# Kernel optimization log

Measured on AMD Instinct MI355X. Metric: run time of the kernel, lower is better.

Reference implementation:

```python
import jax, jax.numpy as jnp
import numpy as np

B = 32; D = 512; NH = 8; DH = 64; DEPTH = 8; MLP = 2048
NC = 256; Hs = 16; Ws = 16; SHIFT = 1
INNER = NH * DH


def setup_inputs() -> dict:
    key = jax.random.key(0)
    ks = jax.random.split(key, 8)
    s = D ** -0.5
    return {
        "z": jax.random.normal(ks[0], (B, D, Hs, Ws), jnp.float32),
        "slots": jax.random.normal(ks[1], (B, NC, D), jnp.float32),
        "pos_emb": jax.random.normal(ks[2], (1, Hs * Ws, D), jnp.float32) * s,
        "slot_pos_emb": jax.random.normal(ks[3], (1, NC, D), jnp.float32) * s,
        "norm_w": jnp.ones((D,), jnp.float32),
        "norm_b": jnp.zeros((D,), jnp.float32),
        "ln1_w": jnp.ones((DEPTH, D), jnp.float32),
        "ln1_b": jnp.zeros((DEPTH, D), jnp.float32),
        "qkv_w": jax.random.normal(ks[4], (DEPTH, D, 3 * INNER), jnp.float32) * 0.02,
        "out_w": jax.random.normal(ks[5], (DEPTH, INNER, D), jnp.float32) * 0.02,
        "out_b": jnp.zeros((DEPTH, D), jnp.float32),
        "ln2_w": jnp.ones((DEPTH, D), jnp.float32),
        "ln2_b": jnp.zeros((DEPTH, D), jnp.float32),
        "mlp_w1": jax.random.normal(ks[6], (DEPTH, D, MLP), jnp.float32) * 0.02,
        "mlp_b1": jnp.zeros((DEPTH, MLP), jnp.float32),
        "mlp_w2": jax.random.normal(ks[7], (DEPTH, MLP, D), jnp.float32) * 0.02,
        "mlp_b2": jnp.zeros((DEPTH, D), jnp.float32),
    }


def _ln(x, w, b):
    m = x.mean(-1, keepdims=True)
    v = ((x - m) ** 2).mean(-1, keepdims=True)
    return (x - m) * jax.lax.rsqrt(v + 1e-5) * w + b


def reference(z, slots, pos_emb, slot_pos_emb, norm_w, norm_b,
              ln1_w, ln1_b, qkv_w, out_w, out_b,
              ln2_w, ln2_b, mlp_w1, mlp_b1, mlp_w2, mlp_b2):
    S = NC + Hs * Ws  # 512 tokens: carriers then patches
    mem = slots + slot_pos_emb                                   # [B, NC, D]
    h = z.reshape(B, D, Hs * Ws).transpose(0, 2, 1) + pos_emb    # [B, HW, D]
    x = jnp.concatenate([mem, h], axis=1)                        # [B, S, D]
    x = _ln(x, norm_w, norm_b)
    causal = jnp.tril(jnp.ones((S, S), dtype=bool))              # allowed positions
    scale = DH ** -0.5
    for i in range(DEPTH):
        y = _ln(x, ln1_w[i], ln1_b[i])
        qkv = y @ qkv_w[i]                                       # [B, S, 3*INNER]
        q, k, v = jnp.split(qkv, 3, axis=-1)
        q = q.reshape(B, S, NH, DH).transpose(0, 2, 1, 3)
        k = k.reshape(B, S, NH, DH).transpose(0, 2, 1, 3)
        v = v.reshape(B, S, NH, DH).transpose(0, 2, 1, 3)
        att = jnp.einsum('bhqd,bhkd->bhqk', q, k) * scale
        att = jnp.where(causal, att, jnp.float32(-1e30))
        att = jax.nn.softmax(att, axis=-1)
        o = jnp.einsum('bhqk,bhkd->bhqd', att, v)
        o = o.transpose(0, 2, 1, 3).reshape(B, S, INNER)
        x = x + o @ out_w[i] + out_b[i]
        y = _ln(x, ln2_w[i], ln2_b[i])
        x = x + jax.nn.gelu(y @ mlp_w1[i] + mlp_b1[i], approximate=False) @ mlp_w2[i] + mlp_b2[i]
    out = x[:, NC - SHIFT:NC - SHIFT + Hs * Ws]                  # shifted slice
    return out.transpose(0, 2, 1).reshape(B, D, Hs, Ws)
```

## Files before the change

kernel.cpp:

```cpp
#include <hip/hip_runtime.h>
#include <hip/hip_bf16.h>
#include <math.h>

#define Bb 32
#define Dd 512
#define Ss 512
#define NHh 8
#define DHh 64
#define MLPm 2048
#define NCc 256
#define INNERi 512
#define Mrows (Bb*Ss)

typedef __bf16 bf16x8 __attribute__((ext_vector_type(8)));
typedef float floatx4 __attribute__((ext_vector_type(4)));

__device__ __forceinline__ void load_lds16(const void* g, void* l) {
  __builtin_amdgcn_global_load_lds(
      (__attribute__((address_space(1))) void*)(g),
      (__attribute__((address_space(3))) void*)(l), 16, 0, 0);
}

__device__ __forceinline__ int swz(int row, int seg) {
  return row * 64 + (((seg) ^ (row & 7)) << 3);
}

__global__ void transpose_w(const float* __restrict__ in, __hip_bfloat16* __restrict__ out,
                            int K, int N, size_t in_ls, size_t out_ls)
{
  __shared__ float tile[32][33];
  in  += (size_t)blockIdx.z * in_ls;
  out += (size_t)blockIdx.z * out_ls;
  int n0 = blockIdx.x * 32, k0 = blockIdx.y * 32;
  int tx = threadIdx.x;
  #pragma unroll
  for (int i = threadIdx.y; i < 32; i += 8)
    tile[i][tx] = in[(size_t)(k0 + i) * N + n0 + tx];
  __syncthreads();
  #pragma unroll
  for (int i = threadIdx.y; i < 32; i += 8)
    out[(size_t)(n0 + i) * K + k0 + tx] = __float2bfloat16(tile[tx][i]);
}

__global__ void prologue_kernel(const float* __restrict__ z, const float* __restrict__ slots,
                                const float* __restrict__ pos, const float* __restrict__ spos,
                                const float* __restrict__ nw, const float* __restrict__ nb,
                                float* __restrict__ x)
{
  int row = blockIdx.x;
  int b = row >> 9, s = row & 511;
  int lane = threadIdx.x;
  float v[8];
  float sum = 0.f;
  #pragma unroll
  for (int j = 0; j < 8; ++j) {
    int d = lane + j * 64;
    float t;
    if (s < NCc) t = slots[((size_t)b * NCc + s) * Dd + d] + spos[(size_t)s * Dd + d];
    else {
      int sp = s - NCc;
      t = z[((size_t)b * Dd + d) * 256 + sp] + pos[(size_t)sp * Dd + d];
    }
    v[j] = t; sum += t;
  }
  #pragma unroll
  for (int o = 32; o; o >>= 1) sum += __shfl_xor(sum, o);
  float mean = sum * (1.f / Dd);
  float vs = 0.f;
  #pragma unroll
  for (int j = 0; j < 8; ++j) { float d = v[j] - mean; vs += d * d; }
  #pragma unroll
  for (int o = 32; o; o >>= 1) vs += __shfl_xor(vs, o);
  float rs = rsqrtf(vs * (1.f / Dd) + 1e-5f);
  #pragma unroll
  for (int j = 0; j < 8; ++j) {
    int d = lane + j * 64;
    x[(size_t)row * Dd + d] = (v[j] - mean) * rs * nw[d] + nb[d];
  }
}

__global__ void ln_kernel(const float* __restrict__ x, const float* __restrict__ w,
                          const float* __restrict__ b, __hip_bfloat16* __restrict__ y)
{
  int row = blockIdx.x * 4 + (threadIdx.x >> 6);
  int lane = threadIdx.x & 63;
  const float* xr = x + (size_t)row * Dd;
  float v[8];
  float sum = 0.f;
  #pragma unroll
  for (int j = 0; j < 8; ++j) { v[j] = xr[lane + j * 64]; sum += v[j]; }
  #pragma unroll
  for (int o = 32; o; o >>= 1) sum += __shfl_xor(sum, o);
  float mean = sum * (1.f / Dd);
  float vs = 0.f;
  #pragma unroll
  for (int j = 0; j < 8; ++j) { float d = v[j] - mean; vs += d * d; }
  #pragma unroll
  for (int o = 32; o; o >>= 1) vs += __shfl_xor(vs, o);
  float rs = rsqrtf(vs * (1.f / Dd) + 1e-5f);
  #pragma unroll
  for (int j = 0; j < 8; ++j) {
    int d = lane + j * 64;
    y[(size_t)row * Dd + d] = __float2bfloat16((v[j] - mean) * rs * w[d] + b[d]);
  }
}

template <int MODE>
__global__ __launch_bounds__(256, 2)
void gemm_bt(const __hip_bfloat16* __restrict__ A, const __hip_bfloat16* __restrict__ Bt,
             const float* __restrict__ bias, const float* __restrict__ res,
             void* __restrict__ Out, int M, int N, int K)
{
  constexpr int BM = 128, BN = 128, BK = 64;
  __shared__ __align__(16) __hip_bfloat16 As[BM * BK];
  __shared__ __align__(16) __hip_bfloat16 Bs[BN * BK];
  const int tid = threadIdx.x;
  const int lane = tid & 63;
  const int wave = tid >> 6;

  const int NBLK = N >> 7;
  const int bid = blockIdx.x;
  const int xcd = bid & 7;
  const int j = bid >> 3;
  const int nb = j % NBLK;
  const int mt = xcd + ((j / NBLK) << 3);
  const int m0 = mt << 7;
  const int n0 = nb << 7;

  const int wm = (wave & 1) * 64;
  const int wn = (wave >> 1) * 64;
  const int quad = lane >> 4;
  const int lrow = lane & 15;

  floatx4 acc[4][4];
  #pragma unroll
  for (int i = 0; i < 4; ++i)
    #pragma unroll
    for (int jj = 0; jj < 4; ++jj) {
      floatx4 z4 = {0.f, 0.f, 0.f, 0.f};
      acc[i][jj] = z4;
    }

  for (int k0 = 0; k0 < K; k0 += BK) {
    #pragma unroll
    for (int it = 0; it < 4; ++it) {
      int c = it * 256 + tid;
      int row = c >> 3, seg = (c & 7) ^ (row & 7);
      load_lds16(A + (size_t)(m0 + row) * K + k0 + seg * 8, As + c * 8);
    }
    #pragma unroll
    for (int it = 0; it < 4; ++it) {
      int c = it * 256 + tid;
      int row = c >> 3, seg = (c & 7) ^ (row & 7);
      load_lds16(Bt + (size_t)(n0 + row) * K + k0 + seg * 8, Bs + c * 8);
    }
    __syncthreads();

    #pragma unroll
    for (int k1 = 0; k1 < BK; k1 += 32) {
      const int s0 = k1 >> 3;
      bf16x8 a[4], b[4];
      #pragma unroll
      for (int i = 0; i < 4; ++i)
        a[i] = *reinterpret_cast<const bf16x8*>(&As[swz(wm + i * 16 + lrow, s0 + quad)]);
      #pragma unroll
      for (int i = 0; i < 4; ++i)
        b[i] = *reinterpret_cast<const bf16x8*>(&Bs[swz(wn + i * 16 + lrow, s0 + quad)]);
      #pragma unroll
      for (int mi = 0; mi < 4; ++mi)
        #pragma unroll
        for (int ni = 0; ni < 4; ++ni)
          acc[mi][ni] = __builtin_amdgcn_mfma_f32_16x16x32_bf16(a[mi], b[ni], acc[mi][ni], 0, 0, 0);
    }
    __syncthreads();
  }

  #pragma unroll
  for (int mi = 0; mi < 4; ++mi) {
    #pragma unroll
    for (int r = 0; r < 4; ++r) {
      int gm = m0 + wm + mi * 16 + quad * 4 + r;
      #pragma unroll
      for (int ni = 0; ni < 4; ++ni) {
        int gn = n0 + wn + ni * 16 + lrow;
        float v = acc[mi][ni][r];
        size_t oi = (size_t)gm * N + gn;
        if (MODE == 0) {
          ((__hip_bfloat16*)Out)[oi] = __float2bfloat16(v);
        } else if (MODE == 1) {
          ((float*)Out)[oi] = v + bias[gn] + res[oi];
        } else {
          float t = v + bias[gn];
          float g = 0.5f * t * (1.0f + erff(t * 0.70710678118654752f));
          ((__hip_bfloat16*)Out)[oi] = __float2bfloat16(g);
        }
      }
    }
  }
}

__global__ __launch_bounds__(256, 2)
void attn_pair(const __hip_bfloat16* __restrict__ qkv, __hip_bfloat16* __restrict__ o)
{
  const int p = blockIdx.x;
  const int h = blockIdx.y, b = blockIdx.z;
  const int t0 = p, t1 = 7 - p;

  __shared__ __align__(16) __hip_bfloat16 Qs[2][64 * 64];
  __shared__ __align__(16) __hip_bfloat16 Ks[64 * 64];
  __shared__ __align__(16) __hip_bfloat16 Vt[64 * 64];
  __shared__ __align__(16) __hip_bfloat16 Ps[4][16 * 64];

  const int tid = threadIdx.x, lane = tid & 63, wave = tid >> 6;
  const int quad = lane >> 4, col = lane & 15;
  const size_t base = ((size_t)b * Ss) * 1536 + (size_t)h * 64;

  #pragma unroll
  for (int t = 0; t < 2; ++t) {
    const int tq = t ? t1 : t0;
    #pragma unroll
    for (int it = 0; it < 2; ++it) {
      int c = it * 256 + tid;
      int row = c >> 3, seg = c & 7;
      bf16x8 q8 = *reinterpret_cast<const bf16x8*>(
          qkv + base + (size_t)(tq * 64 + row) * 1536 + seg * 8);
      *reinterpret_cast<bf16x8*>(&Qs[t][swz(row, seg)]) = q8;
    }
  }

  bf16x8 kreg[2], vreg[2];
  auto load_kv = [&](int c0) {
    #pragma unroll
    for (int it = 0; it < 2; ++it) {
      int c = it * 256 + tid;
      kreg[it] = *reinterpret_cast<const bf16x8*>(
          qkv + base + 512 + (size_t)(c0 * 64 + (c >> 3)) * 1536 + (c & 7) * 8);
    }
    #pragma unroll
    for (int it = 0; it < 2; ++it) {
      int row = tid & 63, seg = it * 4 + wave;
      vreg[it] = *reinterpret_cast<const bf16x8*>(
          qkv + base + 1024 + (size_t)(c0 * 64 + row) * 1536 + seg * 8);
    }
  };
  auto store_kv = [&]() {
    #pragma unroll
    for (int it = 0; it < 2; ++it) {
      int c = it * 256 + tid;
      *reinterpret_cast<bf16x8*>(&Ks[swz(c >> 3, c & 7)]) = kreg[it];
    }
    #pragma unroll
    for (int it = 0; it < 2; ++it) {
      int row = tid & 63, seg = it * 4 + wave;
      union { bf16x8 v; __hip_bfloat16 e[8]; } u; u.v = vreg[it];
      #pragma unroll
      for (int j = 0; j < 8; ++j) {
        int d = seg * 8 + j;
        Vt[d * 64 + ((((row >> 3)) ^ (d & 7)) << 3) + (row & 7)] = u.e[j];
      }
    }
  };

  float  mrow[2][4], lsum[2][4];
  floatx4 accO[2][4];
  #pragma unroll
  for (int t = 0; t < 2; ++t)
    #pragma unroll
    for (int r = 0; r < 4; ++r) {
      mrow[t][r] = -1e30f; lsum[t][r] = 0.f;
      floatx4 z4 = {0.f, 0.f, 0.f, 0.f};
      accO[t][r] = z4;
    }

  auto compute_tile = [&](const __hip_bfloat16* Qt, int tq, int c,
                          float* mr, float* ls, floatx4* aO) {
    floatx4 accS[4];
    #pragma unroll
    for (int i = 0; i < 4; ++i) { floatx4 z4 = {0.f,0.f,0.f,0.f}; accS[i] = z4; }
    const int m = wave * 16 + col;
    #pragma unroll
    for (int kc = 0; kc < 2; ++kc) {
      bf16x8 aq = *reinterpret_cast<const bf16x8*>(&Qt[swz(m, kc * 4 + quad)]);
      #pragma unroll
      for (int ni = 0; ni < 4; ++ni) {
        bf16x8 bk = *reinterpret_cast<const bf16x8*>(&Ks[swz(ni * 16 + col, kc * 4 + quad)]);
        accS[ni] = __builtin_amdgcn_mfma_f32_16x16x32_bf16(aq, bk, accS[ni], 0, 0, 0);
      }
    }

    const bool diag = (c == tq);
    float sc[4][4];
    #pragma unroll
    for (int ni = 0; ni < 4; ++ni)
      #pragma unroll
      for (int r = 0; r < 4; ++r) {
        float s = accS[ni][r] * 0.125f;
        if (diag && (ni * 16 + col) > (wave * 16 + quad * 4 + r)) s = -1e30f;
        sc[ni][r] = s;
      }

    #pragma unroll
    for (int r = 0; r < 4; ++r) {
      float cm = fmaxf(fmaxf(sc[0][r], sc[1][r]), fmaxf(sc[2][r], sc[3][r]));
      #pragma unroll
      for (int off = 1; off < 16; off <<= 1) cm = fmaxf(cm, __shfl_xor(cm, off));
      float mnew = fmaxf(mr[r], cm);
      float alpha = __expf(mr[r] - mnew);
      mr[r] = mnew;
      float ps = 0.f;
      #pragma unroll
      for (int ni = 0; ni < 4; ++ni) {
        float pv = __expf(sc[ni][r] - mnew);
        sc[ni][r] = pv;
        ps += pv;
      }
      #pragma unroll
      for (int off = 1; off < 16; off <<= 1) ps += __shfl_xor(ps, off);
      ls[r] = ls[r] * alpha + ps;
      #pragma unroll
      for (int ni = 0; ni < 4; ++ni) aO[ni][r] *= alpha;
    }

    #pragma unroll
    for (int ni = 0; ni < 4; ++ni)
      #pragma unroll
      for (int r = 0; r < 4; ++r) {
        int prow = quad * 4 + r;
        int pseg = ni * 2 + (col >> 3);
        Ps[wave][prow * 64 + ((pseg ^ (prow & 7)) << 3) + (col & 7)] =
            __float2bfloat16(sc[ni][r]);
      }

    #pragma unroll
    for (int kc = 0; kc < 2; ++kc) {
      bf16x8 ap = *reinterpret_cast<const bf16x8*>(&Ps[wave][swz(col, kc * 4 + quad)]);
      #pragma unroll
      for (int ni = 0; ni < 4; ++ni) {
        bf16x8 bv = *reinterpret_cast<const bf16x8*>(&Vt[swz(ni * 16 + col, kc * 4 + quad)]);
        aO[ni] = __builtin_amdgcn_mfma_f32_16x16x32_bf16(ap, bv, aO[ni], 0, 0, 0);
      }
    }
  };

  load_kv(0);
  for (int c = 0; c <= t1; ++c) {
    __syncthreads();
    store_kv();
    __syncthreads();
    if (c < t1) load_kv(c + 1);
    compute_tile(Qs[1], t1, c, mrow[1], lsum[1], accO[1]);
    if (c <= t0) compute_tile(Qs[0], t0, c, mrow[0], lsum[0], accO[0]);
  }

  #pragma unroll
  for (int t = 0; t < 2; ++t) {
    const int tq = t ? t1 : t0;
    float inv[4];
    #pragma unroll
    for (int r = 0; r < 4; ++r) inv[r] = 1.f / lsum[t][r];
    #pragma unroll
    for (int ni = 0; ni < 4; ++ni)
      #pragma unroll
      for (int r = 0; r < 4; ++r) {
        int qg = tq * 64 + wave * 16 + quad * 4 + r;
        o[((size_t)b * Ss + qg) * INNERi + h * 64 + ni * 16 + col] =
            __float2bfloat16(accO[t][ni][r] * inv[r]);
      }
  }
}

__global__ void epilogue_kernel(const float* __restrict__ x, float* __restrict__ out)
{
  int idx = blockIdx.x * 256 + threadIdx.x;
  int sp = idx & 255;
  int bd = idx >> 8;
  int b = bd >> 9, d = bd & 511;
  out[idx] = x[((size_t)b * Ss + (NCc - 1) + sp) * Dd + d];
}

extern "C" void kernel_launch(void* const* d_in, const int* in_sizes, int n_in,
                              void* d_out, int out_size, void* d_ws, size_t ws_size,
                              hipStream_t stream)
{
  const float* z       = (const float*)d_in[0];
  const float* slots   = (const float*)d_in[1];
  const float* pos_emb = (const float*)d_in[2];
  const float* spos    = (const float*)d_in[3];
  const float* norm_w  = (const float*)d_in[4];
  const float* norm_b  = (const float*)d_in[5];
  const float* ln1_w   = (const float*)d_in[6];
  const float* ln1_b   = (const float*)d_in[7];
  const float* qkv_w   = (const float*)d_in[8];
  const float* out_w   = (const float*)d_in[9];
  const float* out_b   = (const float*)d_in[10];
  const float* ln2_w   = (const float*)d_in[11];
  const float* ln2_b   = (const float*)d_in[12];
  const float* mlp_w1  = (const float*)d_in[13];
  const float* mlp_b1  = (const float*)d_in[14];
  const float* mlp_w2  = (const float*)d_in[15];
  const float* mlp_b2  = (const float*)d_in[16];

  char* ws = (char*)d_ws;
  float*          xbuf = (float*)ws;
  __hip_bfloat16* ybuf = (__hip_bfloat16*)(ws + 33554432);
  __hip_bfloat16* qkvb = (__hip_bfloat16*)(ws + 50331648);
  __hip_bfloat16* obuf = (__hip_bfloat16*)(ws + 100663296);
  __hip_bfloat16* hbuf = (__hip_bfloat16*)(ws + 50331648);
  __hip_bfloat16* wT   = (__hip_bfloat16*)(ws + 117440512);

  const size_t WL = 3145728;

  dim3 tb(32, 8);
  transpose_w<<<dim3(1536 / 32, 512 / 32, 8), tb, 0, stream>>>(qkv_w,  wT + 0,       512, 1536, (size_t)512 * 1536, WL);
  transpose_w<<<dim3(512 / 32,  512 / 32, 8), tb, 0, stream>>>(out_w,  wT + 786432,  512, 512,  (size_t)512 * 512,  WL);
  transpose_w<<<dim3(2048 / 32, 512 / 32, 8), tb, 0, stream>>>(mlp_w1, wT + 1048576, 512, 2048, (size_t)512 * 2048, WL);
  transpose_w<<<dim3(512 / 32, 2048 / 32, 8), tb, 0, stream>>>(mlp_w2, wT + 2097152, 2048, 512, (size_t)2048 * 512, WL);

  prologue_kernel<<<Mrows, 64, 0, stream>>>(z, slots, pos_emb, spos, norm_w, norm_b, xbuf);

  for (int i = 0; i < 8; ++i) {
    const __hip_bfloat16* qkvT = wT + (size_t)i * WL;
    const __hip_bfloat16* outT = wT + (size_t)i * WL + 786432;
    const __hip_bfloat16* w1T  = wT + (size_t)i * WL + 1048576;
    const __hip_bfloat16* w2T  = wT + (size_t)i * WL + 2097152;

    ln_kernel<<<Mrows / 4, 256, 0, stream>>>(xbuf, ln1_w + i * Dd, ln1_b + i * Dd, ybuf);
    gemm_bt<0><<<dim3((1536 / 128) * (Mrows / 128)), 256, 0, stream>>>(
        ybuf, qkvT, nullptr, nullptr, qkvb, Mrows, 1536, 512);
    attn_pair<<<dim3(4, NHh, Bb), 256, 0, stream>>>(qkvb, obuf);
    gemm_bt<1><<<dim3((512 / 128) * (Mrows / 128)), 256, 0, stream>>>(
        obuf, outT, out_b + i * Dd, xbuf, xbuf, Mrows, 512, 512);
    ln_kernel<<<Mrows / 4, 256, 0, stream>>>(xbuf, ln2_w + i * Dd, ln2_b + i * Dd, ybuf);
    gemm_bt<2><<<dim3((2048 / 128) * (Mrows / 128)), 256, 0, stream>>>(
        ybuf, w1T, mlp_b1 + i * MLPm, nullptr, hbuf, Mrows, 2048, 512);
    gemm_bt<1><<<dim3((512 / 128) * (Mrows / 128)), 256, 0, stream>>>(
        hbuf, w2T, mlp_b2 + i * Dd, xbuf, xbuf, Mrows, 512, 2048);
  }

  epilogue_kernel<<<(Bb * Dd * 256) / 256, 256, 0, stream>>>(xbuf, (float*)d_out);
}
```

Measured before the change: 1.903 ms.

## Add 256x256-tile pipelined GEMM for QKV and MLP-up projections

Adds a new 512-thread GEMM kernel with 256x256 output tiles. It double-buffers K-halves in 128KB of dynamic LDS through direct global-to-LDS loads, uses explicit barriers and vmcnt waits to overlap staging with MFMA, and raises wave priority around the MFMA blocks. Blocks are remapped so consecutive tiles share an XCD. The QKV and MLP-up GEMMs use it to raise arithmetic intensity and hide load latency. The price is high register and LDS use, which limits occupancy, and only 384/512 blocks per launch, so wave quantization could hurt.

```diff
diff --git a/kernel.cpp b/kernel.cpp
--- a/kernel.cpp
+++ b/kernel.cpp
@@ -197,6 +197,174 @@
       }
     }
   }
+}
+
+#define GBAR()    asm volatile("s_barrier" ::: "memory")
+#define GWAIT10() asm volatile("s_waitcnt vmcnt(10)" ::: "memory")
+
+template <int MODE>
+__global__ __launch_bounds__(512, 2)
+void gemm256(const __hip_bfloat16* __restrict__ A, const __hip_bfloat16* __restrict__ Bt,
+             const float* __restrict__ bias, void* __restrict__ Out,
+             int M, int N, int K)
+{
+  extern __shared__ __hip_bfloat16 lds[];
+  const int tid  = threadIdx.x;
+  const int lane = tid & 63;
+  const int wave = tid >> 6;
+  const int wm = wave >> 2, wn = wave & 3;
+  const int quad = lane >> 4, lrow = lane & 15;
+
+  const int NBN = N >> 8;
+  const int nwg = gridDim.x;
+  const int bid = blockIdx.x;
+  const int qq = nwg >> 3, rr = nwg & 7;
+  const int xcd = bid & 7, oin = bid >> 3;
+  const int wg = (xcd < rr ? xcd * (qq + 1) : rr * (qq + 1) + (xcd - rr) * qq) + oin;
+  const int m0 = (wg / NBN) << 8;
+  const int n0 = (wg % NBN) << 8;
+  const int NT = K >> 6;
+
+  const int srow = tid >> 2;
+  const int sseg = (tid & 3) ^ ((tid >> 3) & 3);
+  const __hip_bfloat16* gA = A  + (size_t)(m0 + srow) * K + sseg * 8;
+  const __hip_bfloat16* gB = Bt + (size_t)(n0 + srow) * K + sseg * 8;
+  const size_t gstep = (size_t)128 * K;
+
+  __hip_bfloat16* const Abase = lds;
+  __hip_bfloat16* const Bbase = lds + 32768;
+
+  auto stageA = [&](int t, int kh) {
+    int ts = t < NT ? t : NT - 1;
+    int kb = ts * 64 + kh * 32;
+    __hip_bfloat16* d = Abase + ((((t & 1) << 1) | kh) * 8192) + tid * 8;
+    load_lds16(gA + kb, d);
+    load_lds16(gA + gstep + kb, d + 4096);
+  };
+  auto stageB = [&](int t, int kh) {
+    int ts = t < NT ? t : NT - 1;
+    int kb = ts * 64 + kh * 32;
+    __hip_bfloat16* d = Bbase + ((((t & 1) << 1) | kh) * 8192) + tid * 8;
+    load_lds16(gB + kb, d);
+    load_lds16(gB + gstep + kb, d + 4096);
+  };
+
+  floatx4 acc[2][4][4];
+  #pragma unroll
+  for (int mh = 0; mh < 2; ++mh)
+    #pragma unroll
+    for (int mi = 0; mi < 4; ++mi)
+      #pragma unroll
+      for (int ni = 0; ni < 4; ++ni) {
+        floatx4 z4 = {0.f, 0.f, 0.f, 0.f};
+        acc[mh][mi][ni] = z4;
+      }
+
+  const int rseg = ((quad ^ ((lrow >> 1) & 3)) << 3);
+  const int arow = (wm * 128 + lrow) * 32 + rseg;
+  const int brow = (wn * 64 + lrow) * 32 + rseg;
+
+  stageB(0, 0); stageA(0, 0); stageB(0, 1); stageA(0, 1);
+  stageB(1, 0); stageA(1, 0); stageB(1, 1);
+  GWAIT10();
+  GBAR();
+
+  bf16x8 af[4], bfr[4];
+  for (int t = 0; t < NT; ++t) {
+    const int par = t & 1;
+    const __hip_bfloat16* As0 = Abase + ((par << 1) | 0) * 8192;
+    const __hip_bfloat16* As1 = Abase + ((par << 1) | 1) * 8192;
+    const __hip_bfloat16* Bs0 = Bbase + ((par << 1) | 0) * 8192;
+    const __hip_bfloat16* Bs1 = Bbase + ((par << 1) | 1) * 8192;
+
+    #pragma unroll
+    for (int ni = 0; ni < 4; ++ni)
+      bfr[ni] = *reinterpret_cast<const bf16x8*>(Bs0 + brow + ni * 512);
+    #pragma unroll
+    for (int mi = 0; mi < 4; ++mi)
+      af[mi] = *reinterpret_cast<const bf16x8*>(As0 + arow + mi * 512);
+    stageA(t + 1, 1);
+    GBAR();
+    __builtin_amdgcn_s_setprio(1);
+    #pragma unroll
+    for (int mi = 0; mi < 4; ++mi)
+      #pragma unroll
+      for (int ni = 0; ni < 4; ++ni)
+        acc[0][mi][ni] = __builtin_amdgcn_mfma_f32_16x16x32_bf16(af[mi], bfr[ni], acc[0][mi][ni], 0, 0, 0);
+    __builtin_amdgcn_s_setprio(0);
+    GBAR();
+
+    #pragma unroll
+    for (int mi = 0; mi < 4; ++mi)
+      af[mi] = *reinterpret_cast<const bf16x8*>(As0 + arow + 2048 + mi * 512);
+    stageB(t + 2, 0);
+    GBAR();
+    __builtin_amdgcn_s_setprio(1);
+    #pragma unroll
+    for (int mi = 0; mi < 4; ++mi)
+      #pragma unroll
+      for (int ni = 0; ni < 4; ++ni)
+        acc[1][mi][ni] = __builtin_amdgcn_mfma_f32_16x16x32_bf16(af[mi], bfr[ni], acc[1][mi][ni], 0, 0, 0);
+    __builtin_amdgcn_s_setprio(0);
+    GWAIT10();
+    GBAR();
+
+    #pragma unroll
+    for (int ni = 0; ni < 4; ++ni)
+      bfr[ni] = *reinterpret_cast<const bf16x8*>(Bs1 + brow + ni * 512);
+    #pragma unroll
+    for (int mi = 0; mi < 4; ++mi)
+      af[mi] = *reinterpret_cast<const bf16x8*>(As1 + arow + mi * 512);
+    stageA(t + 2, 0);
+    GBAR();
+    __builtin_amdgcn_s_setprio(1);
+    #pragma unroll
+    for (int mi = 0; mi < 4; ++mi)
+      #pragma unroll
+      for (int ni = 0; ni < 4; ++ni)
+        acc[0][mi][ni] = __builtin_amdgcn_mfma_f32_16x16x32_bf16(af[mi], bfr[ni], acc[0][mi][ni], 0, 0, 0);
+    __builtin_amdgcn_s_setprio(0);
+    GBAR();
+
+    #pragma unroll
+    for (int mi = 0; mi < 4; ++mi)
+      af[mi] = *reinterpret_cast<const bf16x8*>(As1 + arow + 2048 + mi * 512);
+    stageB(t + 2, 1);
+    GBAR();
+    __builtin_amdgcn_s_setprio(1);
+    #pragma unroll
+    for (int mi = 0; mi < 4; ++mi)
+      #pragma unroll
+      for (int ni = 0; ni < 4; ++ni)
+        acc[1][mi][ni] = __builtin_amdgcn_mfma_f32_16x16x32_bf16(af[mi], bfr[ni], acc[1][mi][ni], 0, 0, 0);
+    __builtin_amdgcn_s_setprio(0);
+    GWAIT10();
+    GBAR();
+  }
+
+  const int cm0 = m0 + wm * 128 + quad * 4;
+  const int cn0 = n0 + wn * 64 + lrow;
+  #pragma unroll
+  for (int mh = 0; mh < 2; ++mh)
+    #pragma unroll
+    for (int mi = 0; mi < 4; ++mi)
+      #pragma unroll
+      for (int r = 0; r < 4; ++r) {
+        const int gm = cm0 + mh * 64 + mi * 16 + r;
+        #pragma unroll
+        for (int ni = 0; ni < 4; ++ni) {
+          const int gn = cn0 + ni * 16;
+          float v = acc[mh][mi][ni][r];
+          size_t oi = (size_t)gm * N + gn;
+          if (MODE == 0) {
+            ((__hip_bfloat16*)Out)[oi] = __float2bfloat16(v);
+          } else {
+            float tt = v + bias[gn];
+            float g = 0.5f * tt * (1.0f + erff(tt * 0.70710678118654752f));
+            ((__hip_bfloat16*)Out)[oi] = __float2bfloat16(g);
+          }
+        }
+      }
 }
 
 __global__ __launch_bounds__(256, 2)
@@ -410,6 +578,11 @@
 
   const size_t WL = 3145728;
 
+  hipFuncSetAttribute(reinterpret_cast<const void*>(&gemm256<0>),
+                      hipFuncAttributeMaxDynamicSharedMemorySize, 131072);
+  hipFuncSetAttribute(reinterpret_cast<const void*>(&gemm256<2>),
+                      hipFuncAttributeMaxDynamicSharedMemorySize, 131072);
+
   dim3 tb(32, 8);
   transpose_w<<<dim3(1536 / 32, 512 / 32, 8), tb, 0, stream>>>(qkv_w,  wT + 0,       512, 1536, (size_t)512 * 1536, WL);
   transpose_w<<<dim3(512 / 32,  512 / 32, 8), tb, 0, stream>>>(out_w,  wT + 786432,  512, 512,  (size_t)512 * 512,  WL);
@@ -425,14 +598,14 @@
     const __hip_bfloat16* w2T  = wT + (size_t)i * WL + 2097152;
 
     ln_kernel<<<Mrows / 4, 256, 0, stream>>>(xbuf, ln1_w + i * Dd, ln1_b + i * Dd, ybuf);
-    gemm_bt<0><<<dim3((1536 / 128) * (Mrows / 128)), 256, 0, stream>>>(
-        ybuf, qkvT, nullptr, nullptr, qkvb, Mrows, 1536, 512);
+    gemm256<0><<<dim3((1536 / 256) * (Mrows / 256)), 512, 131072, stream>>>(
+        ybuf, qkvT, nullptr, qkvb, Mrows, 1536, 512);
     attn_pair<<<dim3(4, NHh, Bb), 256, 0, stream>>>(qkvb, obuf);
     gemm_bt<1><<<dim3((512 / 128) * (Mrows / 128)), 256, 0, stream>>>(
         obuf, outT, out_b + i * Dd, xbuf, xbuf, Mrows, 512, 512);
     ln_kernel<<<Mrows / 4, 256, 0, stream>>>(xbuf, ln2_w + i * Dd, ln2_b + i * Dd, ybuf);
-    gemm_bt<2><<<dim3((2048 / 128) * (Mrows / 128)), 256, 0, stream>>>(
-        ybuf, w1T, mlp_b1 + i * MLPm, nullptr, hbuf, Mrows, 2048, 512);
+    gemm256<2><<<dim3((2048 / 256) * (Mrows / 256)), 512, 131072, stream>>>(
+        ybuf, w1T, mlp_b1 + i * MLPm, hbuf, Mrows, 2048, 512);
     gemm_bt<1><<<dim3((512 / 128) * (Mrows / 128)), 256, 0, stream>>>(
         hbuf, w2T, mlp_b2 + i * Dd, xbuf, xbuf, Mrows, 512, 2048);
   }
```

Result: slower. 2.111 ms (+10.9%).
